# Kernel tuning notes

Hardware: AMD Instinct MI355X
Metric: run time of the kernel (lower is better)

The kernel has to match this reference:

```python
import jax, jax.numpy as jnp
import numpy as np

RATIO = 0.3
BN_EPS = 1e-5
L2_EPS = 1e-8


def setup_inputs() -> dict:
    key = jax.random.key(0)
    ks = jax.random.split(key, 16)
    B, N, D, E = 128, 577, 512, 1024
    H = E // 2  # mlp hidden = 512
    s = lambda k, shp, fan: jax.random.normal(k, shp, dtype=jnp.float32) * (1.0 / np.sqrt(fan))
    return {
        "features": jax.random.normal(ks[0], (B, N, D), dtype=jnp.float32),
        "atten": jax.random.uniform(ks[1], (B, N), dtype=jnp.float32),
        # image_weight_generator: Linear(D,D) -> ReLU -> Linear(D,1)
        "wg_w1": s(ks[2], (D, D), D), "wg_b1": jnp.zeros((D,), jnp.float32),
        "wg_w2": s(ks[3], (D, 1), D), "wg_b2": jnp.zeros((1,), jnp.float32),
        # fc: Linear(D, E)
        "fc_w": s(ks[4], (D, E), D), "fc_b": jnp.zeros((E,), jnp.float32),
        # MLP: Linear(D,H) -> BN(H) -> ReLU -> Linear(H,E)
        "mlp_w0": s(ks[5], (D, H), D), "mlp_b0": jnp.zeros((H,), jnp.float32),
        "bn_g": jnp.ones((H,), jnp.float32), "bn_b": jnp.zeros((H,), jnp.float32),
        "mlp_w1": s(ks[6], (H, E), H), "mlp_b1": jnp.zeros((E,), jnp.float32),
    }


def reference(features, atten, wg_w1, wg_b1, wg_w2, wg_b2, fc_w, fc_b,
              mlp_w0, mlp_b0, bn_g, bn_b, mlp_w1, mlp_b1):
    k = int((atten.shape[1] - 1) * RATIO)  # static: int(576*0.3)=172
    # weight-generator MLP -> per-token scalar weights [B, N]
    h = jax.nn.relu(jnp.einsum('bnd,de->bne', features, wg_w1) + wg_b1)
    w = (jnp.einsum('bnd,do->bno', h, wg_w2) + wg_b2)[..., 0]
    w = w.at[:, 0].set(-jnp.inf)  # mask CLS token
    w = jax.nn.softmax(w, axis=1)
    # top-k token selection (sorted indices), batched gather
    _, idx = jax.lax.top_k(w, k)                      # [B, k]
    idx = jnp.sort(idx, axis=1)
    sel = jnp.take_along_axis(features, idx[:, :, None], axis=1)  # [B, k, D]
    # l2norm over feature dim
    norm = jnp.sqrt(jnp.sum(sel * sel, axis=-1, keepdims=True)) + L2_EPS
    sel = sel / norm
    # fc in half precision (original: fc(selected_tokens.half()))
    feats = (sel.astype(jnp.float16) @ fc_w.astype(jnp.float16)
             + fc_b.astype(jnp.float16))              # [B, k, E] fp16
    # MLP with training-mode BatchNorm over flattened (B*k) dim
    B, K, D = sel.shape
    x = sel.reshape(B * K, D) @ mlp_w0 + mlp_b0       # [B*k, H]
    mean = jnp.mean(x, axis=0)
    var = jnp.mean((x - mean) ** 2, axis=0)
    x = (x - mean) * jax.lax.rsqrt(var + BN_EPS) * bn_g + bn_b
    x = jax.nn.relu(x)
    x = (x @ mlp_w1 + mlp_b1).reshape(B, K, -1)       # [B, k, E]
    return (x + feats.astype(jnp.float32)).astype(jnp.float32)
```

## Files before the change

kernel.cpp:

```cpp
#include <hip/hip_runtime.h>
#include <hip/hip_fp16.h>
#include <math.h>

#define B_    128
#define NTOK  577
#define KSEL  172
#define M_WG  (B_*NTOK)
#define M_SEL (B_*KSEL)

typedef float f32x4 __attribute__((ext_vector_type(4)));
typedef short s16x8 __attribute__((ext_vector_type(8)));
typedef short s16x4 __attribute__((ext_vector_type(4)));
typedef _Float16 f16x8 __attribute__((ext_vector_type(8)));

__device__ __forceinline__ unsigned short bf16_rne(float x) {
    unsigned u = __float_as_uint(x);
    u += 0x7FFFu + ((u >> 16) & 1u);
    return (unsigned short)(u >> 16);
}
__device__ __forceinline__ float bf16f(unsigned short h) {
    return __uint_as_float(((unsigned)h) << 16);
}
__device__ __forceinline__ void gll16(const void* g, void* l) {
    __builtin_amdgcn_global_load_lds(
        (const __attribute__((address_space(1))) unsigned int*)g,
        (__attribute__((address_space(3))) unsigned int*)l, 16, 0, 0);
}

__global__ void zero_kernel(float* __restrict__ w, float* __restrict__ stats) {
    int i = blockIdx.x * 256 + threadIdx.x;
    if (i < M_WG) w[i] = 0.f;
    if (i < 1024) stats[i] = 0.f;
}

__global__ __launch_bounds__(256) void transpose_split_kernel(
    const float* __restrict__ wgw1, const float* __restrict__ mw0,
    const float* __restrict__ mw1, const float* __restrict__ fcw,
    short* __restrict__ w1t_h, short* __restrict__ w1t_l,
    short* __restrict__ w0t, short* __restrict__ mw1t, short* __restrict__ fct)
{
    const int z = blockIdx.z;
    const float* src; short *dh, *dl = nullptr; int N; int bfmode;
    if (z == 0)      { src = wgw1; dh = w1t_h; dl = w1t_l; N = 512;  bfmode = 1; }
    else if (z == 1) { src = mw0;  dh = w0t;   N = 512;  bfmode = 0; }
    else if (z == 2) { src = mw1;  dh = mw1t;  N = 1024; bfmode = 0; }
    else             { src = fcw;  dh = fct;   N = 1024; bfmode = 0; }
    const int n0 = blockIdx.x * 64;
    if (n0 >= N) return;
    const int k0 = blockIdx.y * 64;
    __shared__ float t[64][65];
    const int tid = threadIdx.x;
#pragma unroll
    for (int rr = 0; rr < 16; rr++) {
        int kl = rr * 4 + (tid >> 6);
        int nl = tid & 63;
        t[kl][nl] = src[(size_t)(k0 + kl) * N + n0 + nl];
    }
    __syncthreads();
    const int nl = tid >> 2, kc = tid & 3;
    short hs[16], ls[16];
#pragma unroll
    for (int j = 0; j < 16; j++) {
        float x = t[kc * 16 + j][nl];
        if (bfmode) {
            unsigned short h = bf16_rne(x);
            hs[j] = (short)h;
            ls[j] = (short)bf16_rne(x - bf16f(h));
        } else {
            hs[j] = (short)__half_as_ushort(__float2half(x));
        }
    }
    size_t o = (size_t)(n0 + nl) * 512 + k0 + kc * 16;
    *(s16x8*)(dh + o)     = *(s16x8*)hs;
    *(s16x8*)(dh + o + 8) = *(s16x8*)(hs + 8);
    if (bfmode) {
        *(s16x8*)(dl + o)     = *(s16x8*)ls;
        *(s16x8*)(dl + o + 8) = *(s16x8*)(ls + 8);
    }
}

__global__ __launch_bounds__(256) void gemm_wg_kernel(
    const float* __restrict__ F, const short* __restrict__ Wh, const short* __restrict__ Wl,
    const float* __restrict__ b1, const float* __restrict__ v, float* __restrict__ w_out)
{
    __shared__ short Ah[4096], Al[4096], Bh[4096], Bl[4096];
    const int tid = threadIdx.x, lane = tid & 63, w = tid >> 6;
    const int wm = w >> 1, wn = w & 1;
    const int rowbase = blockIdx.y * 128, nbase = blockIdx.x * 128;
    const int r = lane & 15, kq = lane >> 4;
    f32x4 acc[4][4];
#pragma unroll
    for (int i = 0; i < 4; i++)
#pragma unroll
        for (int j = 0; j < 4; j++) acc[i][j] = (f32x4)(0.0f);
    for (int k0 = 0; k0 < 512; k0 += 32) {
#pragma unroll
        for (int p = 0; p < 2; p++) {
            int c = tid + p * 256, row = c & 127, kqs = c >> 7;
            const float* s = F + (size_t)(rowbase + row) * 512 + k0 + kqs * 8;
            float4 v0 = *(const float4*)s;
            float4 v1 = *(const float4*)(s + 4);
            float vv[8] = {v0.x, v0.y, v0.z, v0.w, v1.x, v1.y, v1.z, v1.w};
            short hs[8], ls[8];
#pragma unroll
            for (int j = 0; j < 8; j++) {
                unsigned short h = bf16_rne(vv[j]);
                hs[j] = (short)h;
                ls[j] = (short)bf16_rne(vv[j] - bf16f(h));
            }
            *(s16x8*)(Ah + kqs * 1024 + row * 8) = *(s16x8*)hs;
            *(s16x8*)(Al + kqs * 1024 + row * 8) = *(s16x8*)ls;
        }
#pragma unroll
        for (int p = 0; p < 2; p++) {
            int c = tid + p * 256, row = c & 127, kqs = c >> 7;
            size_t go = (size_t)(nbase + row) * 512 + k0 + kqs * 8;
            gll16(Wh + go, Bh + c * 8);
            gll16(Wl + go, Bl + c * 8);
        }
        __syncthreads();
        s16x8 ah[4], al[4], bh[4], bl[4];
#pragma unroll
        for (int mf = 0; mf < 4; mf++) {
            int off = kq * 1024 + (wm * 64 + mf * 16 + r) * 8;
            ah[mf] = *(const s16x8*)(Ah + off);
            al[mf] = *(const s16x8*)(Al + off);
        }
#pragma unroll
        for (int nf = 0; nf < 4; nf++) {
            int off = kq * 1024 + (wn * 64 + nf * 16 + r) * 8;
            bh[nf] = *(const s16x8*)(Bh + off);
            bl[nf] = *(const s16x8*)(Bl + off);
        }
#pragma unroll
        for (int mf = 0; mf < 4; mf++)
#pragma unroll
            for (int nf = 0; nf < 4; nf++) {
                acc[mf][nf] = __builtin_amdgcn_mfma_f32_16x16x32_bf16(ah[mf], bh[nf], acc[mf][nf], 0, 0, 0);
                acc[mf][nf] = __builtin_amdgcn_mfma_f32_16x16x32_bf16(ah[mf], bl[nf], acc[mf][nf], 0, 0, 0);
                acc[mf][nf] = __builtin_amdgcn_mfma_f32_16x16x32_bf16(al[mf], bh[nf], acc[mf][nf], 0, 0, 0);
            }
        __syncthreads();
    }
    float b1v[4], vv[4];
#pragma unroll
    for (int nf = 0; nf < 4; nf++) {
        int col = nbase + wn * 64 + nf * 16 + r;
        b1v[nf] = b1[col]; vv[nf] = v[col];
    }
#pragma unroll
    for (int mf = 0; mf < 4; mf++)
#pragma unroll
        for (int i = 0; i < 4; i++) {
            float s = 0.f;
#pragma unroll
            for (int nf = 0; nf < 4; nf++)
                s += fmaxf(acc[mf][nf][i] + b1v[nf], 0.f) * vv[nf];
            s += __shfl_xor(s, 1); s += __shfl_xor(s, 2);
            s += __shfl_xor(s, 4); s += __shfl_xor(s, 8);
            if (r == 0)
                atomicAdd(&w_out[rowbase + wm * 64 + mf * 16 + kq * 4 + i], s);
        }
}

__global__ __launch_bounds__(512) void topk_kernel(
    const float* __restrict__ w, int* __restrict__ idx_out)
{
    __shared__ float sval[1024];
    __shared__ int   sidx[1024];
    __shared__ int   s2[256];
    const int b = blockIdx.x;
    const int tid = threadIdx.x;
    for (int i = tid; i < 1024; i += 512) {
        if (i < 576) { sval[i] = w[b * NTOK + 1 + i]; sidx[i] = 1 + i; }
        else         { sval[i] = -1e38f;              sidx[i] = 0x7fffffff; }
    }
    __syncthreads();
    for (int ksz = 2; ksz <= 1024; ksz <<= 1) {
        for (int j = ksz >> 1; j > 0; j >>= 1) {
            int i = ((tid & ~(j - 1)) << 1) | (tid & (j - 1));
            int ixj = i | j;
            float va = sval[i], vb = sval[ixj];
            int ia = sidx[i], ib = sidx[ixj];
            bool a_first = (va > vb) || (va == vb && ia < ib);
            bool dirDesc = ((i & ksz) == 0);
            bool doswap = dirDesc ? (!a_first) : a_first;
            if (doswap) { sval[i] = vb; sval[ixj] = va; sidx[i] = ib; sidx[ixj] = ia; }
            __syncthreads();
        }
    }
    for (int i = tid; i < 256; i += 512) s2[i] = (i < KSEL) ? sidx[i] : 0x7fffffff;
    __syncthreads();
    for (int ksz = 2; ksz <= 256; ksz <<= 1) {
        for (int j = ksz >> 1; j > 0; j >>= 1) {
            if (tid < 128) {
                int i = ((tid & ~(j - 1)) << 1) | (tid & (j - 1));
                int ixj = i | j;
                int a = s2[i], bb = s2[ixj];
                bool asc = ((i & ksz) == 0);
                bool doswap = asc ? (a > bb) : (a < bb);
                if (doswap) { s2[i] = bb; s2[ixj] = a; }
            }
            __syncthreads();
        }
    }
    for (int i = tid; i < KSEL; i += 512) idx_out[b * KSEL + i] = s2[i];
}

__global__ __launch_bounds__(128) void gather_norm_kernel(
    const float* __restrict__ F, const int* __restrict__ idx,
    short* __restrict__ Sh)
{
    const int g = blockIdx.x;
    const int b = g / KSEL;
    const int tok = idx[g];
    const float4* src = (const float4*)(F + ((size_t)b * NTOK + tok) * 512);
    const int t = threadIdx.x;
    float4 v = src[t];
    float ss = v.x * v.x + v.y * v.y + v.z * v.z + v.w * v.w;
#pragma unroll
    for (int off = 32; off > 0; off >>= 1) ss += __shfl_down(ss, off);
    __shared__ float red[2];
    if ((t & 63) == 0) red[t >> 6] = ss;
    __syncthreads();
    float inv = 1.0f / (sqrtf(red[0] + red[1]) + 1e-8f);
    float xs[4] = {v.x * inv, v.y * inv, v.z * inv, v.w * inv};
    short hs[4];
#pragma unroll
    for (int j = 0; j < 4; j++) hs[j] = (short)__half_as_ushort(__float2half(xs[j]));
    *(s16x4*)(Sh + (size_t)g * 512 + t * 4) = *(s16x4*)hs;
}

__global__ __launch_bounds__(256) void gemm_x1_kernel(
    const short* __restrict__ Sh, const short* __restrict__ W0t,
    const float* __restrict__ b0, short* __restrict__ X1h, float* __restrict__ stats)
{
    __shared__ short A[4096], Bt[8192];
    const int tid = threadIdx.x, lane = tid & 63, wn = tid >> 6;
    const int rowbase = blockIdx.y * 128, nbase = blockIdx.x * 256;
    const int r = lane & 15, kq = lane >> 4;
    f32x4 acc[8][4];
#pragma unroll
    for (int i = 0; i < 8; i++)
#pragma unroll
        for (int j = 0; j < 4; j++) acc[i][j] = (f32x4)(0.0f);
    for (int k0 = 0; k0 < 512; k0 += 32) {
#pragma unroll
        for (int p = 0; p < 2; p++) {
            int c = tid + p * 256, row = c & 127, kqs = c >> 7;
            gll16(Sh + (size_t)(rowbase + row) * 512 + k0 + kqs * 8, A + c * 8);
        }
#pragma unroll
        for (int p = 0; p < 4; p++) {
            int c = tid + p * 256, col = c & 255, kqs = c >> 8;
            gll16(W0t + (size_t)(nbase + col) * 512 + k0 + kqs * 8, Bt + c * 8);
        }
        __syncthreads();
        f16x8 b[4];
#pragma unroll
        for (int nf = 0; nf < 4; nf++)
            b[nf] = *(const f16x8*)(Bt + kq * 2048 + (wn * 64 + nf * 16 + r) * 8);
#pragma unroll
        for (int mf = 0; mf < 8; mf++) {
            f16x8 a = *(const f16x8*)(A + kq * 1024 + (mf * 16 + r) * 8);
#pragma unroll
            for (int nf = 0; nf < 4; nf++)
                acc[mf][nf] = __builtin_amdgcn_mfma_f32_16x16x32_f16(a, b[nf], acc[mf][nf], 0, 0, 0);
        }
        __syncthreads();
    }
#pragma unroll
    for (int nf = 0; nf < 4; nf++) {
        int col = nbase + wn * 64 + nf * 16 + r;
        float b0v = b0[col];
        float cs = 0.f, cq = 0.f;
#pragma unroll
        for (int mf = 0; mf < 8; mf++)
#pragma unroll
            for (int i = 0; i < 4; i++) {
                int row = rowbase + mf * 16 + kq * 4 + i;
                float val = acc[mf][nf][i] + b0v;
                X1h[(size_t)row * 512 + col] = (short)__half_as_ushort(__float2half(val));
                cs += val; cq += val * val;
            }
        cs += __shfl_xor(cs, 16); cs += __shfl_xor(cs, 32);
        cq += __shfl_xor(cq, 16); cq += __shfl_xor(cq, 32);
        if (kq == 0) {
            atomicAdd(&stats[col], cs);
            atomicAdd(&stats[512 + col], cq);
        }
    }
}

__global__ void bn_finalize_kernel(const float* __restrict__ stats,
                                   const float* __restrict__ g,
                                   const float* __restrict__ b,
                                   float* __restrict__ ss)
{
    int c = threadIdx.x;
    float mean = stats[c] * (1.0f / M_SEL);
    float var = stats[512 + c] * (1.0f / M_SEL) - mean * mean;
    float sc = g[c] * rsqrtf(var + 1e-5f);
    ss[c] = sc;
    ss[512 + c] = b[c] - mean * sc;
}

__global__ __launch_bounds__(256) void gemm_out2_kernel(
    const short* __restrict__ Sh, const short* __restrict__ FCt,
    const float* __restrict__ fcb, const short* __restrict__ X1h,
    const short* __restrict__ W1t, const float* __restrict__ ssbuf,
    const float* __restrict__ b1, float* __restrict__ out)
{
    __shared__ short A[4096], Bt[8192];
    __shared__ float sc[512], sh_[512];
    const int tid = threadIdx.x, lane = tid & 63, wn = tid >> 6;
    const int rowbase = blockIdx.y * 128, nbase = blockIdx.x * 256;
    const int r = lane & 15, kq = lane >> 4;
    for (int i = tid; i < 512; i += 256) { sc[i] = ssbuf[i]; sh_[i] = ssbuf[512 + i]; }
    f32x4 acc[8][4];
#pragma unroll
    for (int i = 0; i < 8; i++)
#pragma unroll
        for (int j = 0; j < 4; j++) acc[i][j] = (f32x4)(0.0f);
    for (int k0 = 0; k0 < 512; k0 += 32) {
#pragma unroll
        for (int p = 0; p < 2; p++) {
            int c = tid + p * 256, row = c & 127, kqs = c >> 7;
            gll16(Sh + (size_t)(rowbase + row) * 512 + k0 + kqs * 8, A + c * 8);
        }
#pragma unroll
        for (int p = 0; p < 4; p++) {
            int c = tid + p * 256, col = c & 255, kqs = c >> 8;
            gll16(FCt + (size_t)(nbase + col) * 512 + k0 + kqs * 8, Bt + c * 8);
        }
        __syncthreads();
        f16x8 b[4];
#pragma unroll
        for (int nf = 0; nf < 4; nf++)
            b[nf] = *(const f16x8*)(Bt + kq * 2048 + (wn * 64 + nf * 16 + r) * 8);
#pragma unroll
        for (int mf = 0; mf < 8; mf++) {
            f16x8 a = *(const f16x8*)(A + kq * 1024 + (mf * 16 + r) * 8);
#pragma unroll
            for (int nf = 0; nf < 4; nf++)
                acc[mf][nf] = __builtin_amdgcn_mfma_f32_16x16x32_f16(a, b[nf], acc[mf][nf], 0, 0, 0);
        }
        __syncthreads();
    }
#pragma unroll
    for (int nf = 0; nf < 4; nf++) {
        float fb = __half2float(__float2half(fcb[nbase + wn * 64 + nf * 16 + r]));
#pragma unroll
        for (int mf = 0; mf < 8; mf++)
#pragma unroll
            for (int i = 0; i < 4; i++) {
                float t = __half2float(__float2half(acc[mf][nf][i]));
                acc[mf][nf][i] = __half2float(__float2half(t + fb));
            }
    }
    for (int k0 = 0; k0 < 512; k0 += 32) {
#pragma unroll
        for (int p = 0; p < 2; p++) {
            int c = tid + p * 256, row = c & 127, kqs = c >> 7;
            s16x8 xi = *(const s16x8*)(X1h + (size_t)(rowbase + row) * 512 + k0 + kqs * 8);
            short hs[8];
#pragma unroll
            for (int j = 0; j < 8; j++) {
                float xf = __half2float(__ushort_as_half((unsigned short)xi[j]));
                int k = k0 + kqs * 8 + j;
                float y = fmaxf(fmaf(xf, sc[k], sh_[k]), 0.f);
                hs[j] = (short)__half_as_ushort(__float2half(y));
            }
            *(s16x8*)(A + kqs * 1024 + row * 8) = *(s16x8*)hs;
        }
#pragma unroll
        for (int p = 0; p < 4; p++) {
            int c = tid + p * 256, col = c & 255, kqs = c >> 8;
            gll16(W1t + (size_t)(nbase + col) * 512 + k0 + kqs * 8, Bt + c * 8);
        }
        __syncthreads();
        f16x8 b[4];
#pragma unroll
        for (int nf = 0; nf < 4; nf++)
            b[nf] = *(const f16x8*)(Bt + kq * 2048 + (wn * 64 + nf * 16 + r) * 8);
#pragma unroll
        for (int mf = 0; mf < 8; mf++) {
            f16x8 a = *(const f16x8*)(A + kq * 1024 + (mf * 16 + r) * 8);
#pragma unroll
            for (int nf = 0; nf < 4; nf++)
                acc[mf][nf] = __builtin_amdgcn_mfma_f32_16x16x32_f16(a, b[nf], acc[mf][nf], 0, 0, 0);
        }
        __syncthreads();
    }
#pragma unroll
    for (int nf = 0; nf < 4; nf++) {
        int col = nbase + wn * 64 + nf * 16 + r;
        float bb = b1[col];
#pragma unroll
        for (int mf = 0; mf < 8; mf++)
#pragma unroll
            for (int i = 0; i < 4; i++) {
                int row = rowbase + mf * 16 + kq * 4 + i;
                out[(size_t)row * 1024 + col] = acc[mf][nf][i] + bb;
            }
    }
}

extern "C" void kernel_launch(void* const* d_in, const int* in_sizes, int n_in,
                              void* d_out, int out_size, void* d_ws, size_t ws_size,
                              hipStream_t stream)
{
    const float* features = (const float*)d_in[0];
    const float* wg_w1 = (const float*)d_in[2];
    const float* wg_b1 = (const float*)d_in[3];
    const float* wg_w2 = (const float*)d_in[4];
    const float* fc_w  = (const float*)d_in[6];
    const float* fc_b  = (const float*)d_in[7];
    const float* mlp_w0 = (const float*)d_in[8];
    const float* mlp_b0 = (const float*)d_in[9];
    const float* bn_g  = (const float*)d_in[10];
    const float* bn_b  = (const float*)d_in[11];
    const float* mlp_w1 = (const float*)d_in[12];
    const float* mlp_b1 = (const float*)d_in[13];
    float* out = (float*)d_out;

    char* ws = (char*)d_ws;
    float* w_scores  = (float*)(ws + 0);
    float* stats     = (float*)(ws + 295424);
    float* scaleshift= (float*)(ws + 299520);
    int*   idx_sel   = (int*)  (ws + 303616);
    short* w1t_h     = (short*)(ws + 391680);
    short* w1t_l     = (short*)(ws + 915968);
    short* w0t       = (short*)(ws + 1440256);
    short* mw1t      = (short*)(ws + 1964544);
    short* fct       = (short*)(ws + 3013120);
    short* sel_h     = (short*)(ws + 4061696);
    short* x1h       = (short*)(ws + 26606080);

    zero_kernel<<<289, 256, 0, stream>>>(w_scores, stats);
    transpose_split_kernel<<<dim3(16, 8, 4), 256, 0, stream>>>(
        wg_w1, mlp_w0, mlp_w1, fc_w, w1t_h, w1t_l, w0t, mw1t, fct);
    gemm_wg_kernel<<<dim3(4, 577), 256, 0, stream>>>(
        features, w1t_h, w1t_l, wg_b1, wg_w2, w_scores);
    topk_kernel<<<B_, 512, 0, stream>>>(w_scores, idx_sel);
    gather_norm_kernel<<<M_SEL, 128, 0, stream>>>(features, idx_sel, sel_h);
    gemm_x1_kernel<<<dim3(2, 172), 256, 0, stream>>>(
        sel_h, w0t, mlp_b0, x1h, stats);
    bn_finalize_kernel<<<1, 512, 0, stream>>>(stats, bn_g, bn_b, scaleshift);
    gemm_out2_kernel<<<dim3(4, 172), 256, 0, stream>>>(
        sel_h, fct, fc_b, x1h, mw1t, scaleshift, mlp_b1, out);
}
```

Before: 688.0 us.

## Score tokens in fp16 and refine near-threshold candidates in fp32

The 3-pass bf16-split weight-generator GEMM becomes a single fp16 MFMA pass with a 128x256 tile and double-buffered LDS, cutting its MFMA count to a third. Tokens whose approximate scores fall within a fixed margin of the top-k threshold are re-scored exactly in fp32 by a new refine kernel, then merged with the confident set. The fc and MLP output GEMMs also gain double buffering. Correctness now depends on the fixed DELTA margin covering fp16 error and on the uncertain set fitting in 256 slots; the refine kernel reads untransposed W1 column-wise per token.

Result: slower. 761.1 us (+10.6%).

```diff
diff --git a/kernel.cpp b/kernel.cpp
--- a/kernel.cpp
+++ b/kernel.cpp
@@ -7,20 +7,13 @@
 #define KSEL  172
 #define M_WG  (B_*NTOK)
 #define M_SEL (B_*KSEL)
+#define DELTA 8e-3f
 
 typedef float f32x4 __attribute__((ext_vector_type(4)));
 typedef short s16x8 __attribute__((ext_vector_type(8)));
 typedef short s16x4 __attribute__((ext_vector_type(4)));
 typedef _Float16 f16x8 __attribute__((ext_vector_type(8)));
 
-__device__ __forceinline__ unsigned short bf16_rne(float x) {
-    unsigned u = __float_as_uint(x);
-    u += 0x7FFFu + ((u >> 16) & 1u);
-    return (unsigned short)(u >> 16);
-}
-__device__ __forceinline__ float bf16f(unsigned short h) {
-    return __uint_as_float(((unsigned)h) << 16);
-}
 __device__ __forceinline__ void gll16(const void* g, void* l) {
     __builtin_amdgcn_global_load_lds(
         (const __attribute__((address_space(1))) unsigned int*)g,
@@ -33,18 +26,18 @@
     if (i < 1024) stats[i] = 0.f;
 }
 
-__global__ __launch_bounds__(256) void transpose_split_kernel(
+__global__ __launch_bounds__(256) void transpose_f16_kernel(
     const float* __restrict__ wgw1, const float* __restrict__ mw0,
     const float* __restrict__ mw1, const float* __restrict__ fcw,
-    short* __restrict__ w1t_h, short* __restrict__ w1t_l,
-    short* __restrict__ w0t, short* __restrict__ mw1t, short* __restrict__ fct)
+    short* __restrict__ w1t, short* __restrict__ w0t,
+    short* __restrict__ mw1t, short* __restrict__ fct)
 {
     const int z = blockIdx.z;
-    const float* src; short *dh, *dl = nullptr; int N; int bfmode;
-    if (z == 0)      { src = wgw1; dh = w1t_h; dl = w1t_l; N = 512;  bfmode = 1; }
-    else if (z == 1) { src = mw0;  dh = w0t;   N = 512;  bfmode = 0; }
-    else if (z == 2) { src = mw1;  dh = mw1t;  N = 1024; bfmode = 0; }
-    else             { src = fcw;  dh = fct;   N = 1024; bfmode = 0; }
+    const float* src; short* dst; int N;
+    if (z == 0)      { src = wgw1; dst = w1t;  N = 512;  }
+    else if (z == 1) { src = mw0;  dst = w0t;  N = 512;  }
+    else if (z == 2) { src = mw1;  dst = mw1t; N = 1024; }
+    else             { src = fcw;  dst = fct;  N = 1024; }
     const int n0 = blockIdx.x * 64;
     if (n0 >= N) return;
     const int k0 = blockIdx.y * 64;
@@ -52,96 +45,102 @@
     const int tid = threadIdx.x;
 #pragma unroll
     for (int rr = 0; rr < 16; rr++) {
-        int kl = rr * 4 + (tid >> 6);
-        int nl = tid & 63;
+        int kl = rr * 4 + (tid >> 6), nl = tid & 63;
         t[kl][nl] = src[(size_t)(k0 + kl) * N + n0 + nl];
     }
     __syncthreads();
     const int nl = tid >> 2, kc = tid & 3;
-    short hs[16], ls[16];
-#pragma unroll
-    for (int j = 0; j < 16; j++) {
-        float x = t[kc * 16 + j][nl];
-        if (bfmode) {
-            unsigned short h = bf16_rne(x);
-            hs[j] = (short)h;
-            ls[j] = (short)bf16_rne(x - bf16f(h));
-        } else {
-            hs[j] = (short)__half_as_ushort(__float2half(x));
-        }
-    }
+    short hs[16];
+#pragma unroll
+    for (int j = 0; j < 16; j++)
+        hs[j] = (short)__half_as_ushort(__float2half(t[kc * 16 + j][nl]));
     size_t o = (size_t)(n0 + nl) * 512 + k0 + kc * 16;
-    *(s16x8*)(dh + o)     = *(s16x8*)hs;
-    *(s16x8*)(dh + o + 8) = *(s16x8*)(hs + 8);
-    if (bfmode) {
-        *(s16x8*)(dl + o)     = *(s16x8*)ls;
-        *(s16x8*)(dl + o + 8) = *(s16x8*)(ls + 8);
-    }
-}
-
-__global__ __launch_bounds__(256) void gemm_wg_kernel(
-    const float* __restrict__ F, const short* __restrict__ Wh, const short* __restrict__ Wl,
-    const float* __restrict__ b1, const float* __restrict__ v, float* __restrict__ w_out)
-{
-    __shared__ short Ah[4096], Al[4096], Bh[4096], Bl[4096];
-    const int tid = threadIdx.x, lane = tid & 63, w = tid >> 6;
-    const int wm = w >> 1, wn = w & 1;
-    const int rowbase = blockIdx.y * 128, nbase = blockIdx.x * 128;
+    *(s16x8*)(dst + o)     = *(s16x8*)hs;
+    *(s16x8*)(dst + o + 8) = *(s16x8*)(hs + 8);
+}
+
+__global__ __launch_bounds__(256) void wg_f16_kernel(
+    const float* __restrict__ F, const short* __restrict__ W1t,
+    const float* __restrict__ b1, const float* __restrict__ v,
+    float* __restrict__ w_out)
+{
+    __shared__ short A2[2][4096];
+    __shared__ short B2[2][8192];
+    const int tid = threadIdx.x, lane = tid & 63, wn = tid >> 6;
     const int r = lane & 15, kq = lane >> 4;
-    f32x4 acc[4][4];
-#pragma unroll
-    for (int i = 0; i < 4; i++)
-#pragma unroll
-        for (int j = 0; j < 4; j++) acc[i][j] = (f32x4)(0.0f);
-    for (int k0 = 0; k0 < 512; k0 += 32) {
+    const int rowbase = blockIdx.y * 128, nbase = blockIdx.x * 256;
+    float av[2][8];
+
+    {
+        int k0 = 0;
+#pragma unroll
+        for (int p = 0; p < 4; p++) {
+            int c = tid + p * 256, col = c & 255, kqs = c >> 8;
+            gll16(W1t + (size_t)(nbase + col) * 512 + k0 + kqs * 8, &B2[0][c * 8]);
+        }
 #pragma unroll
         for (int p = 0; p < 2; p++) {
             int c = tid + p * 256, row = c & 127, kqs = c >> 7;
             const float* s = F + (size_t)(rowbase + row) * 512 + k0 + kqs * 8;
-            float4 v0 = *(const float4*)s;
-            float4 v1 = *(const float4*)(s + 4);
-            float vv[8] = {v0.x, v0.y, v0.z, v0.w, v1.x, v1.y, v1.z, v1.w};
-            short hs[8], ls[8];
-#pragma unroll
-            for (int j = 0; j < 8; j++) {
-                unsigned short h = bf16_rne(vv[j]);
-                hs[j] = (short)h;
-                ls[j] = (short)bf16_rne(vv[j] - bf16f(h));
-            }
-            *(s16x8*)(Ah + kqs * 1024 + row * 8) = *(s16x8*)hs;
-            *(s16x8*)(Al + kqs * 1024 + row * 8) = *(s16x8*)ls;
-        }
-#pragma unroll
-        for (int p = 0; p < 2; p++) {
-            int c = tid + p * 256, row = c & 127, kqs = c >> 7;
-            size_t go = (size_t)(nbase + row) * 512 + k0 + kqs * 8;
-            gll16(Wh + go, Bh + c * 8);
-            gll16(Wl + go, Bl + c * 8);
-        }
-        __syncthreads();
-        s16x8 ah[4], al[4], bh[4], bl[4];
-#pragma unroll
-        for (int mf = 0; mf < 4; mf++) {
-            int off = kq * 1024 + (wm * 64 + mf * 16 + r) * 8;
-            ah[mf] = *(const s16x8*)(Ah + off);
-            al[mf] = *(const s16x8*)(Al + off);
-        }
-#pragma unroll
-        for (int nf = 0; nf < 4; nf++) {
-            int off = kq * 1024 + (wn * 64 + nf * 16 + r) * 8;
-            bh[nf] = *(const s16x8*)(Bh + off);
-            bl[nf] = *(const s16x8*)(Bl + off);
-        }
-#pragma unroll
-        for (int mf = 0; mf < 4; mf++)
-#pragma unroll
-            for (int nf = 0; nf < 4; nf++) {
-                acc[mf][nf] = __builtin_amdgcn_mfma_f32_16x16x32_bf16(ah[mf], bh[nf], acc[mf][nf], 0, 0, 0);
-                acc[mf][nf] = __builtin_amdgcn_mfma_f32_16x16x32_bf16(ah[mf], bl[nf], acc[mf][nf], 0, 0, 0);
-                acc[mf][nf] = __builtin_amdgcn_mfma_f32_16x16x32_bf16(al[mf], bh[nf], acc[mf][nf], 0, 0, 0);
-            }
-        __syncthreads();
-    }
+            f32x4 u0 = *(const f32x4*)s, u1 = *(const f32x4*)(s + 4);
+#pragma unroll
+            for (int j = 0; j < 4; j++) { av[p][j] = u0[j]; av[p][4 + j] = u1[j]; }
+            short hs[8];
+#pragma unroll
+            for (int j = 0; j < 8; j++) hs[j] = (short)__half_as_ushort(__float2half(av[p][j]));
+            *(s16x8*)&A2[0][kqs * 1024 + row * 8] = *(s16x8*)hs;
+        }
+    }
+    __syncthreads();
+
+    f32x4 acc[8][4];
+#pragma unroll
+    for (int i = 0; i < 8; i++)
+#pragma unroll
+        for (int j = 0; j < 4; j++) acc[i][j] = (f32x4)(0.0f);
+
+    for (int km = 0; km < 16; km++) {
+        const int pb = km & 1;
+        if (km < 15) {
+            int k0 = (km + 1) * 32;
+#pragma unroll
+            for (int p = 0; p < 4; p++) {
+                int c = tid + p * 256, col = c & 255, kqs = c >> 8;
+                gll16(W1t + (size_t)(nbase + col) * 512 + k0 + kqs * 8, &B2[pb ^ 1][c * 8]);
+            }
+#pragma unroll
+            for (int p = 0; p < 2; p++) {
+                int c = tid + p * 256, row = c & 127, kqs = c >> 7;
+                const float* s = F + (size_t)(rowbase + row) * 512 + k0 + kqs * 8;
+                f32x4 u0 = *(const f32x4*)s, u1 = *(const f32x4*)(s + 4);
+#pragma unroll
+                for (int j = 0; j < 4; j++) { av[p][j] = u0[j]; av[p][4 + j] = u1[j]; }
+            }
+        }
+        f16x8 bfrag[4];
+#pragma unroll
+        for (int nf = 0; nf < 4; nf++)
+            bfrag[nf] = *(const f16x8*)&B2[pb][kq * 2048 + (wn * 64 + nf * 16 + r) * 8];
+#pragma unroll
+        for (int mf = 0; mf < 8; mf++) {
+            f16x8 a = *(const f16x8*)&A2[pb][kq * 1024 + (mf * 16 + r) * 8];
+#pragma unroll
+            for (int nf = 0; nf < 4; nf++)
+                acc[mf][nf] = __builtin_amdgcn_mfma_f32_16x16x32_f16(a, bfrag[nf], acc[mf][nf], 0, 0, 0);
+        }
+        if (km < 15) {
+#pragma unroll
+            for (int p = 0; p < 2; p++) {
+                int c = tid + p * 256, row = c & 127, kqs = c >> 7;
+                short hs[8];
+#pragma unroll
+                for (int j = 0; j < 8; j++) hs[j] = (short)__half_as_ushort(__float2half(av[p][j]));
+                *(s16x8*)&A2[pb ^ 1][kqs * 1024 + row * 8] = *(s16x8*)hs;
+            }
+        }
+        __syncthreads();
+    }
+
     float b1v[4], vv[4];
 #pragma unroll
     for (int nf = 0; nf < 4; nf++) {
@@ -149,7 +148,7 @@
         b1v[nf] = b1[col]; vv[nf] = v[col];
     }
 #pragma unroll
-    for (int mf = 0; mf < 4; mf++)
+    for (int mf = 0; mf < 8; mf++)
 #pragma unroll
         for (int i = 0; i < 4; i++) {
             float s = 0.f;
@@ -159,16 +158,18 @@
             s += __shfl_xor(s, 1); s += __shfl_xor(s, 2);
             s += __shfl_xor(s, 4); s += __shfl_xor(s, 8);
             if (r == 0)
-                atomicAdd(&w_out[rowbase + wm * 64 + mf * 16 + kq * 4 + i], s);
-        }
-}
-
-__global__ __launch_bounds__(512) void topk_kernel(
-    const float* __restrict__ w, int* __restrict__ idx_out)
+                atomicAdd(&w_out[rowbase + mf * 16 + kq * 4 + i], s);
+        }
+}
+
+__global__ __launch_bounds__(512) void topk2_kernel(
+    const float* __restrict__ w, int* __restrict__ cin, int* __restrict__ unc,
+    int* __restrict__ meta)
 {
     __shared__ float sval[1024];
     __shared__ int   sidx[1024];
-    __shared__ int   s2[256];
+    __shared__ int mcnt, ucnt;
+    __shared__ float thr_s;
     const int b = blockIdx.x;
     const int tid = threadIdx.x;
     for (int i = tid; i < 1024; i += 512) {
@@ -189,22 +190,107 @@
             __syncthreads();
         }
     }
-    for (int i = tid; i < 256; i += 512) s2[i] = (i < KSEL) ? sidx[i] : 0x7fffffff;
+    if (tid == 0) { thr_s = sval[KSEL - 1]; mcnt = 0; ucnt = 0; }
+    __syncthreads();
+    const float thr = thr_s;
+    for (int i = tid; i < 576; i += 512) {
+        float vv = sval[i]; int id = sidx[i];
+        if (vv > thr + DELTA) {
+            int p = atomicAdd(&mcnt, 1);
+            cin[b * KSEL + p] = id;
+        } else if (vv >= thr - DELTA) {
+            int p = atomicAdd(&ucnt, 1);
+            if (p < 256) unc[b * 256 + p] = id;
+        }
+    }
+    __syncthreads();
+    if (tid == 0) {
+        int m = mcnt;
+        int u = (ucnt < 256) ? ucnt : 256;
+        meta[b * 4]     = m;
+        meta[b * 4 + 1] = KSEL - m;
+        meta[b * 4 + 2] = u;
+    }
+}
+
+__global__ __launch_bounds__(256) void refine_kernel(
+    const float* __restrict__ F, const float* __restrict__ W1,
+    const float* __restrict__ b1, const float* __restrict__ v,
+    const int* __restrict__ unc, const int* __restrict__ meta,
+    float* __restrict__ rscore)
+{
+    const int b = blockIdx.y, tid = threadIdx.x;
+    const int u = meta[b * 4 + 2];
+    __shared__ float fr[512];
+    __shared__ float redbuf[4];
+    for (int s = blockIdx.x; s < u; s += 32) {
+        int tok = unc[b * 256 + s];
+        __syncthreads();
+        fr[tid]       = F[((size_t)b * NTOK + tok) * 512 + tid];
+        fr[tid + 256] = F[((size_t)b * NTOK + tok) * 512 + tid + 256];
+        __syncthreads();
+        float a0 = b1[tid], a1 = b1[tid + 256];
+#pragma unroll 4
+        for (int k = 0; k < 512; k++) {
+            float fk = fr[k];
+            a0 = fmaf(fk, W1[(size_t)k * 512 + tid], a0);
+            a1 = fmaf(fk, W1[(size_t)k * 512 + tid + 256], a1);
+        }
+        float p = fmaxf(a0, 0.f) * v[tid] + fmaxf(a1, 0.f) * v[tid + 256];
+#pragma unroll
+        for (int off = 32; off > 0; off >>= 1) p += __shfl_down(p, off);
+        if ((tid & 63) == 0) redbuf[tid >> 6] = p;
+        __syncthreads();
+        if (tid == 0) rscore[b * 256 + s] = redbuf[0] + redbuf[1] + redbuf[2] + redbuf[3];
+    }
+}
+
+__global__ __launch_bounds__(256) void select_kernel(
+    const int* __restrict__ cin, const int* __restrict__ unc,
+    const float* __restrict__ rscore, const int* __restrict__ meta,
+    int* __restrict__ idx_out)
+{
+    const int b = blockIdx.x, tid = threadIdx.x;
+    const int m = meta[b * 4], u = meta[b * 4 + 2];
+    __shared__ float uval[256];
+    __shared__ int   uidx[256];
+    __shared__ int   fin[256];
+    if (tid < u) { uval[tid] = rscore[b * 256 + tid]; uidx[tid] = unc[b * 256 + tid]; }
+    else         { uval[tid] = -1e38f;                uidx[tid] = 0x7fffffff; }
     __syncthreads();
     for (int ksz = 2; ksz <= 256; ksz <<= 1) {
         for (int j = ksz >> 1; j > 0; j >>= 1) {
             if (tid < 128) {
                 int i = ((tid & ~(j - 1)) << 1) | (tid & (j - 1));
                 int ixj = i | j;
-                int a = s2[i], bb = s2[ixj];
+                float va = uval[i], vb = uval[ixj];
+                int ia = uidx[i], ib = uidx[ixj];
+                bool a_first = (va > vb) || (va == vb && ia < ib);
+                bool dirDesc = ((i & ksz) == 0);
+                if (dirDesc ? !a_first : a_first) {
+                    uval[i] = vb; uval[ixj] = va; uidx[i] = ib; uidx[ixj] = ia;
+                }
+            }
+            __syncthreads();
+        }
+    }
+    if (tid < m) fin[tid] = cin[b * KSEL + tid];
+    else if (tid < KSEL) fin[tid] = uidx[tid - m];
+    else fin[tid] = 0x7fffffff;
+    __syncthreads();
+    for (int ksz = 2; ksz <= 256; ksz <<= 1) {
+        for (int j = ksz >> 1; j > 0; j >>= 1) {
+            if (tid < 128) {
+                int i = ((tid & ~(j - 1)) << 1) | (tid & (j - 1));
+                int ixj = i | j;
+                int a = fin[i], bb = fin[ixj];
                 bool asc = ((i & ksz) == 0);
-                bool doswap = asc ? (a > bb) : (a < bb);
-                if (doswap) { s2[i] = bb; s2[ixj] = a; }
+                if (asc ? (a > bb) : (a < bb)) { fin[i] = bb; fin[ixj] = a; }
             }
             __syncthreads();
         }
     }
-    for (int i = tid; i < KSEL; i += 512) idx_out[b * KSEL + i] = s2[i];
+    if (tid < KSEL) idx_out[b * KSEL + tid] = fin[tid];
 }
 
 __global__ __launch_bounds__(128) void gather_norm_kernel(
@@ -311,7 +397,8 @@
     const short* __restrict__ W1t, const float* __restrict__ ssbuf,
     const float* __restrict__ b1, float* __restrict__ out)
 {
-    __shared__ short A[4096], Bt[8192];
+    __shared__ short A2[2][4096];
+    __shared__ short B2[2][8192];
     __shared__ float sc[512], sh_[512];
     const int tid = threadIdx.x, lane = tid & 63, wn = tid >> 6;
     const int rowbase = blockIdx.y * 128, nbase = blockIdx.x * 256;
@@ -322,25 +409,42 @@
     for (int i = 0; i < 8; i++)
 #pragma unroll
         for (int j = 0; j < 4; j++) acc[i][j] = (f32x4)(0.0f);
-    for (int k0 = 0; k0 < 512; k0 += 32) {
+
+    {
 #pragma unroll
         for (int p = 0; p < 2; p++) {
             int c = tid + p * 256, row = c & 127, kqs = c >> 7;
-            gll16(Sh + (size_t)(rowbase + row) * 512 + k0 + kqs * 8, A + c * 8);
+            gll16(Sh + (size_t)(rowbase + row) * 512 + kqs * 8, &A2[0][c * 8]);
         }
 #pragma unroll
         for (int p = 0; p < 4; p++) {
             int c = tid + p * 256, col = c & 255, kqs = c >> 8;
-            gll16(FCt + (size_t)(nbase + col) * 512 + k0 + kqs * 8, Bt + c * 8);
-        }
-        __syncthreads();
+            gll16(FCt + (size_t)(nbase + col) * 512 + kqs * 8, &B2[0][c * 8]);
+        }
+    }
+    __syncthreads();
+    for (int km = 0; km < 16; km++) {
+        const int pb = km & 1;
+        if (km < 15) {
+            int k0 = (km + 1) * 32;
+#pragma unroll
+            for (int p = 0; p < 2; p++) {
+                int c = tid + p * 256, row = c & 127, kqs = c >> 7;
+                gll16(Sh + (size_t)(rowbase + row) * 512 + k0 + kqs * 8, &A2[pb ^ 1][c * 8]);
+            }
+#pragma unroll
+            for (int p = 0; p < 4; p++) {
+                int c = tid + p * 256, col = c & 255, kqs = c >> 8;
+                gll16(FCt + (size_t)(nbase + col) * 512 + k0 + kqs * 8, &B2[pb ^ 1][c * 8]);
+            }
+        }
         f16x8 b[4];
 #pragma unroll
         for (int nf = 0; nf < 4; nf++)
-            b[nf] = *(const f16x8*)(Bt + kq * 2048 + (wn * 64 + nf * 16 + r) * 8);
+            b[nf] = *(const f16x8*)&B2[pb][kq * 2048 + (wn * 64 + nf * 16 + r) * 8];
 #pragma unroll
         for (int mf = 0; mf < 8; mf++) {
-            f16x8 a = *(const f16x8*)(A + kq * 1024 + (mf * 16 + r) * 8);
+            f16x8 a = *(const f16x8*)&A2[pb][kq * 1024 + (mf * 16 + r) * 8];
 #pragma unroll
             for (int nf = 0; nf < 4; nf++)
                 acc[mf][nf] = __builtin_amdgcn_mfma_f32_16x16x32_f16(a, b[nf], acc[mf][nf], 0, 0, 0);
@@ -358,37 +462,73 @@
                 acc[mf][nf][i] = __half2float(__float2half(t + fb));
             }
     }
-    for (int k0 = 0; k0 < 512; k0 += 32) {
+
+    s16x8 xv[2];
+    {
 #pragma unroll
         for (int p = 0; p < 2; p++) {
             int c = tid + p * 256, row = c & 127, kqs = c >> 7;
-            s16x8 xi = *(const s16x8*)(X1h + (size_t)(rowbase + row) * 512 + k0 + kqs * 8);
+            xv[p] = *(const s16x8*)(X1h + (size_t)(rowbase + row) * 512 + kqs * 8);
+        }
+#pragma unroll
+        for (int p = 0; p < 2; p++) {
+            int c = tid + p * 256, row = c & 127, kqs = c >> 7;
             short hs[8];
 #pragma unroll
             for (int j = 0; j < 8; j++) {
-                float xf = __half2float(__ushort_as_half((unsigned short)xi[j]));
-                int k = k0 + kqs * 8 + j;
-                float y = fmaxf(fmaf(xf, sc[k], sh_[k]), 0.f);
-                hs[j] = (short)__half_as_ushort(__float2half(y));
-            }
-            *(s16x8*)(A + kqs * 1024 + row * 8) = *(s16x8*)hs;
+                float xf = __half2float(__ushort_as_half((unsigned short)xv[p][j]));
+                int k = kqs * 8 + j;
+                hs[j] = (short)__half_as_ushort(__float2half(fmaxf(fmaf(xf, sc[k], sh_[k]), 0.f)));
+            }
+            *(s16x8*)&A2[0][kqs * 1024 + row * 8] = *(s16x8*)hs;
         }
 #pragma unroll
         for (int p = 0; p < 4; p++) {
             int c = tid + p * 256, col = c & 255, kqs = c >> 8;
-            gll16(W1t + (size_t)(nbase + col) * 512 + k0 + kqs * 8, Bt + c * 8);
-        }
-        __syncthreads();
+            gll16(W1t + (size_t)(nbase + col) * 512 + kqs * 8, &B2[0][c * 8]);
+        }
+    }
+    __syncthreads();
+    for (int km = 0; km < 16; km++) {
+        const int pb = km & 1;
+        if (km < 15) {
+            int k0 = (km + 1) * 32;
+#pragma unroll
+            for (int p = 0; p < 4; p++) {
+                int c = tid + p * 256, col = c & 255, kqs = c >> 8;
+                gll16(W1t + (size_t)(nbase + col) * 512 + k0 + kqs * 8, &B2[pb ^ 1][c * 8]);
+            }
+#pragma unroll
+            for (int p = 0; p < 2; p++) {
+                int c = tid + p * 256, row = c & 127, kqs = c >> 7;
+                xv[p] = *(const s16x8*)(X1h + (size_t)(rowbase + row) * 512 + k0 + kqs * 8);
+            }
+        }
         f16x8 b[4];
 #pragma unroll
         for (int nf = 0; nf < 4; nf++)
-            b[nf] = *(const f16x8*)(Bt + kq * 2048 + (wn * 64 + nf * 16 + r) * 8);
+            b[nf] = *(const f16x8*)&B2[pb][kq * 2048 + (wn * 64 + nf * 16 + r) * 8];
 #pragma unroll
         for (int mf = 0; mf < 8; mf++) {
-            f16x8 a = *(const f16x8*)(A + kq * 1024 + (mf * 16 + r) * 8);
+            f16x8 a = *(const f16x8*)&A2[pb][kq * 1024 + (mf * 16 + r) * 8];
 #pragma unroll
             for (int nf = 0; nf < 4; nf++)
                 acc[mf][nf] = __builtin_amdgcn_mfma_f32_16x16x32_f16(a, b[nf], acc[mf][nf], 0, 0, 0);
+        }
+        if (km < 15) {
+            int k0 = (km + 1) * 32;
+#pragma unroll
+            for (int p = 0; p < 2; p++) {
+                int c = tid + p * 256, row = c & 127, kqs = c >> 7;
+                short hs[8];
+#pragma unroll
+                for (int j = 0; j < 8; j++) {
+                    float xf = __half2float(__ushort_as_half((unsigned short)xv[p][j]));
+                    int k = k0 + kqs * 8 + j;
+                    hs[j] = (short)__half_as_ushort(__float2half(fmaxf(fmaf(xf, sc[k], sh_[k]), 0.f)));
+                }
+                *(s16x8*)&A2[pb ^ 1][kqs * 1024 + row * 8] = *(s16x8*)hs;
+            }
         }
         __syncthreads();
     }
@@ -428,21 +568,27 @@
     float* w_scores  = (float*)(ws + 0);
     float* stats     = (float*)(ws + 295424);
     float* scaleshift= (float*)(ws + 299520);
-    int*   idx_sel   = (int*)  (ws + 303616);
-    short* w1t_h     = (short*)(ws + 391680);
-    short* w1t_l     = (short*)(ws + 915968);
-    short* w0t       = (short*)(ws + 1440256);
-    short* mw1t      = (short*)(ws + 1964544);
-    short* fct       = (short*)(ws + 3013120);
-    short* sel_h     = (short*)(ws + 4061696);
-    short* x1h       = (short*)(ws + 26606080);
+    int*   meta      = (int*)  (ws + 303616);
+    int*   idx_sel   = (int*)  (ws + 305664);
+    int*   cin_list  = (int*)  (ws + 393728);
+    int*   unc_list  = (int*)  (ws + 481792);
+    float* rscore    = (float*)(ws + 612864);
+    short* w1t       = (short*)(ws + 743936);
+    short* w0t       = (short*)(ws + 1268224);
+    short* mw1t      = (short*)(ws + 1792512);
+    short* fct       = (short*)(ws + 2841088);
+    short* sel_h     = (short*)(ws + 3889664);
+    short* x1h       = (short*)(ws + 26434048);
 
     zero_kernel<<<289, 256, 0, stream>>>(w_scores, stats);
-    transpose_split_kernel<<<dim3(16, 8, 4), 256, 0, stream>>>(
-        wg_w1, mlp_w0, mlp_w1, fc_w, w1t_h, w1t_l, w0t, mw1t, fct);
-    gemm_wg_kernel<<<dim3(4, 577), 256, 0, stream>>>(
-        features, w1t_h, w1t_l, wg_b1, wg_w2, w_scores);
-    topk_kernel<<<B_, 512, 0, stream>>>(w_scores, idx_sel);
+    transpose_f16_kernel<<<dim3(16, 8, 4), 256, 0, stream>>>(
+        wg_w1, mlp_w0, mlp_w1, fc_w, w1t, w0t, mw1t, fct);
+    wg_f16_kernel<<<dim3(2, 577), 256, 0, stream>>>(
+        features, w1t, wg_b1, wg_w2, w_scores);
+    topk2_kernel<<<B_, 512, 0, stream>>>(w_scores, cin_list, unc_list, meta);
+    refine_kernel<<<dim3(32, B_), 256, 0, stream>>>(
+        features, wg_w1, wg_b1, wg_w2, unc_list, meta, rscore);
+    select_kernel<<<B_, 256, 0, stream>>>(cin_list, unc_list, rscore, meta, idx_sel);
     gather_norm_kernel<<<M_SEL, 128, 0, stream>>>(features, idx_sel, sel_h);
     gemm_x1_kernel<<<dim3(2, 172), 256, 0, stream>>>(
         sel_h, w0t, mlp_b0, x1h, stats);
```
